# Kernel tuning notes

Measured on AMD Instinct MI355X. Metric: run time of the kernel, lower is better.

The kernel has to match this reference:

```python
import jax, jax.numpy as jnp
import numpy as np

B, P, D_IN = 128, 4096, 4   # frames, points/frame, xyz+time
NG = 16                      # number of trajectory groups
H1, H2, H3 = 64, 128, 512    # PointNet shared-MLP widths


def _init_mlp(key, dims):
    ks = jax.random.split(key, len(dims) - 1)
    params = []
    for k, (di, do) in zip(ks, zip(dims[:-1], dims[1:])):
        W = jax.random.normal(k, (di, do), dtype=jnp.float32) * (1.0 / np.sqrt(di))
        b = jnp.zeros((do,), dtype=jnp.float32)
        params.append((W, b))
    return params


def setup_inputs() -> dict:
    key = jax.random.key(0)
    k_pc, k_t, k_idx, k_g, k_l = jax.random.split(key, 5)
    pc = jax.random.normal(k_pc, (B, 3, P), dtype=jnp.float32)
    traj_time_batch = jax.random.uniform(k_t, (B, 1), dtype=jnp.float32)
    traj_inbatch_index = jnp.sort(jax.random.randint(k_idx, (B,), 0, NG)).astype(jnp.int32)
    (Wg1, bg1), (Wg2, bg2), (Wg3, bg3) = _init_mlp(k_g, [D_IN, H1, H2, H3])
    (Wl1, bl1), (Wl2, bl2), (Wl3, bl3) = _init_mlp(k_l, [D_IN, H1, H2, H3])
    return dict(pc=pc, traj_time_batch=traj_time_batch, traj_inbatch_index=traj_inbatch_index,
                Wg1=Wg1, bg1=bg1, Wg2=Wg2, bg2=bg2, Wg3=Wg3, bg3=bg3,
                Wl1=Wl1, bl1=bl1, Wl2=Wl2, bl2=bl2, Wl3=Wl3, bl3=bl3)


def _mlp(x, layers):
    # pointwise shared MLP: x [..., P, d_in] -> [..., P, d_out]
    for W, b in layers:
        x = jax.nn.relu(x @ W + b)
    return x


def reference(pc, traj_time_batch, traj_inbatch_index,
              Wg1, bg1, Wg2, bg2, Wg3, bg3,
              Wl1, bl1, Wl2, bl2, Wl3, bl3):
    b, _, p = pc.shape
    # append time channel: [B,3,P] + [B,1,P] -> [B,4,P]
    t = jnp.broadcast_to(traj_time_batch[..., None], (b, 1, p))
    feat = jnp.concatenate([pc, t], axis=1)
    x = jnp.swapaxes(feat, 1, 2)  # [B,P,4] points-last layout for pointwise MLP

    # global branch: shared MLP on every point, then max over all points of each trajectory group
    hg = _mlp(x, [(Wg1, bg1), (Wg2, bg2), (Wg3, bg3)])           # [B,P,H3]
    seg = jnp.repeat(traj_inbatch_index, p)                       # [B*P]
    gmax = jax.ops.segment_max(hg.reshape(b * p, -1), seg, num_segments=NG)  # [NG,H3]
    global_feat = gmax[traj_inbatch_index]                        # [B,H3] broadcast back per frame

    # local branch: per-frame PointNet encode (shared MLP + max over points)
    hl = _mlp(x, [(Wl1, bl1), (Wl2, bl2), (Wl3, bl3)])            # [B,P,H3]
    local_feat = hl.max(axis=1)                                   # [B,H3]

    z = jnp.concatenate([global_feat, local_feat], axis=1)        # [B,2*H3]
    input_features_vis = pc                                       # original pc (last dim == 4096, no slice)
    return (z, input_features_vis)
```

## Files before the change

### kernel.cpp

```cpp
#include <hip/hip_runtime.h>
#include <hip/hip_bf16.h>

#define NB   128
#define NP   4096
#define NGRP 16
#define C3   512

typedef __bf16 bf16x8 __attribute__((ext_vector_type(8)));
typedef __bf16 bf16x4 __attribute__((ext_vector_type(4)));
typedef float  f32x4  __attribute__((ext_vector_type(4)));

#define WS_W1T_G 0
#define WS_W1T_L 4096
#define WS_W2T_G 8192
#define WS_W2T_L 24576
#define WS_W3T_G 40960
#define WS_W3T_L 172032
#define WS_GMAX  303104

#define H1_S 72
#define H2_S 136

__global__ void prep_kernel(const float* __restrict__ Wg1, const float* __restrict__ Wg2,
                            const float* __restrict__ Wg3, const float* __restrict__ Wl1,
                            const float* __restrict__ Wl2, const float* __restrict__ Wl3,
                            float* __restrict__ out, char* __restrict__ ws) {
    int gid = blockIdx.x * blockDim.x + threadIdx.x;
    out[gid] = 0.0f;
    float* gmax = (float*)(ws + WS_GMAX);
    if (gid < NGRP * C3) gmax[gid] = 0.0f;
    __bf16* w1tg = (__bf16*)(ws + WS_W1T_G);
    __bf16* w1tl = (__bf16*)(ws + WS_W1T_L);
    __bf16* w2tg = (__bf16*)(ws + WS_W2T_G);
    __bf16* w2tl = (__bf16*)(ws + WS_W2T_L);
    __bf16* w3tg = (__bf16*)(ws + WS_W3T_G);
    __bf16* w3tl = (__bf16*)(ws + WS_W3T_L);
    if (gid < 64 * 32) {
        int ch = gid >> 5, k = gid & 31;
        w1tg[gid] = (k < 4) ? (__bf16)Wg1[k * 64 + ch] : (__bf16)0.0f;
        w1tl[gid] = (k < 4) ? (__bf16)Wl1[k * 64 + ch] : (__bf16)0.0f;
    }
    if (gid < 128 * 64) {
        int ch = gid >> 6, k = gid & 63;
        w2tg[gid] = (__bf16)Wg2[k * 128 + ch];
        w2tl[gid] = (__bf16)Wl2[k * 128 + ch];
    }
    if (gid < 512 * 128) {
        int ch = gid >> 7, k = gid & 127;
        w3tg[gid] = (__bf16)Wg3[k * 512 + ch];
        w3tl[gid] = (__bf16)Wl3[k * 512 + ch];
    }
}

__global__ __launch_bounds__(512, 2) void main_kernel(
    const float* __restrict__ pc, const float* __restrict__ tt, const int* __restrict__ idx,
    const float* __restrict__ bg1, const float* __restrict__ bg2, const float* __restrict__ bg3,
    const float* __restrict__ bl1, const float* __restrict__ bl2, const float* __restrict__ bl3,
    float* __restrict__ out, char* __restrict__ ws) {
    __shared__ __align__(16) char smem[78848];
    __bf16* h1 = (__bf16*)smem;
    __bf16* h2 = (__bf16*)(smem + 9216);

    const int tid    = threadIdx.x;
    const int lane   = tid & 63;
    const int wave   = tid >> 6;
    const int quad   = lane >> 4;
    const int l15    = lane & 15;
    const int branch = blockIdx.y;
    const int chunk  = blockIdx.x;
    const int frame  = chunk >> 2;
    const int p0     = (chunk & 3) * 1024;

    const __bf16* w1t = (const __bf16*)(ws + (branch ? WS_W1T_L : WS_W1T_G));
    const __bf16* w2t = (const __bf16*)(ws + (branch ? WS_W2T_L : WS_W2T_G));
    const __bf16* w3t = (const __bf16*)(ws + (branch ? WS_W3T_L : WS_W3T_G));
    const float* b1 = branch ? bl1 : bg1;
    const float* b2 = branch ? bl2 : bg2;
    const float* b3 = branch ? bl3 : bg3;

    const int ni1  = wave >> 1;
    const int mi1  = (wave & 1) * 2;
    const int chb2 = wave * 16;
    const int ch3  = wave * 64;

    bf16x8 a1[2];
    #pragma unroll
    for (int mm = 0; mm < 2; ++mm)
        a1[mm] = *(const bf16x8*)(w1t + ((mi1 + mm) * 16 + l15) * 32 + quad * 8);
    bf16x8 a2[2];
    #pragma unroll
    for (int ks = 0; ks < 2; ++ks)
        a2[ks] = *(const bf16x8*)(w2t + (chb2 + l15) * 64 + ks * 32 + quad * 8);
    bf16x8 aw[4][4];
    #pragma unroll
    for (int mi = 0; mi < 4; ++mi)
        #pragma unroll
        for (int ks = 0; ks < 4; ++ks)
            aw[mi][ks] = *(const bf16x8*)(w3t + (ch3 + mi * 16 + l15) * 128 + ks * 32 + quad * 8);

    float b1r[2][4], b2r[4];
    #pragma unroll
    for (int mm = 0; mm < 2; ++mm)
        #pragma unroll
        for (int r = 0; r < 4; ++r) b1r[mm][r] = b1[(mi1 + mm) * 16 + quad * 4 + r];
    #pragma unroll
    for (int r = 0; r < 4; ++r) b2r[r] = b2[chb2 + quad * 4 + r];

    const float tval = tt[frame];
    const f32x4 zf = {0.0f, 0.0f, 0.0f, 0.0f};
    f32x4 runmax[4];
    #pragma unroll
    for (int mi = 0; mi < 4; ++mi) runmax[mi] = (f32x4){-1e30f, -1e30f, -1e30f, -1e30f};

    const float* pcx = pc + (size_t)frame * 3 * NP;

    for (int m = 0; m < 4; ++m) {
        float xf[4][3];
        const int pb = p0 + m * 256 + ni1 * 16 + l15;
        #pragma unroll
        for (int s = 0; s < 4; ++s) {
            xf[s][0] = pcx[pb + s * 64];
            xf[s][1] = pcx[NP + pb + s * 64];
            xf[s][2] = pcx[2 * NP + pb + s * 64];
        }

        #pragma unroll
        for (int s = 0; s < 4; ++s) {
            bf16x8 xb;
            #pragma unroll
            for (int j = 0; j < 8; ++j) xb[j] = (__bf16)0.0f;
            if (quad == 0) {
                xb[0] = (__bf16)xf[s][0]; xb[1] = (__bf16)xf[s][1];
                xb[2] = (__bf16)xf[s][2]; xb[3] = (__bf16)tval;
            }
            #pragma unroll
            for (int mm = 0; mm < 2; ++mm) {
                f32x4 c = __builtin_amdgcn_mfma_f32_16x16x32_bf16(a1[mm], xb, zf, 0, 0, 0);
                bf16x4 pk;
                #pragma unroll
                for (int r = 0; r < 4; ++r) pk[r] = (__bf16)fmaxf(c[r] + b1r[mm][r], 0.0f);
                *(bf16x4*)(h1 + (ni1 * 16 + l15) * H1_S + (mi1 + mm) * 16 + quad * 4) = pk;
            }
            __syncthreads();
            #pragma unroll
            for (int ni = 0; ni < 4; ++ni) {
                bf16x8 q0 = *(const bf16x8*)(h1 + (ni * 16 + l15) * H1_S + quad * 8);
                bf16x8 q1 = *(const bf16x8*)(h1 + (ni * 16 + l15) * H1_S + 32 + quad * 8);
                f32x4 c = __builtin_amdgcn_mfma_f32_16x16x32_bf16(a2[0], q0, zf, 0, 0, 0);
                c = __builtin_amdgcn_mfma_f32_16x16x32_bf16(a2[1], q1, c, 0, 0, 0);
                bf16x4 pk;
                #pragma unroll
                for (int r = 0; r < 4; ++r) pk[r] = (__bf16)fmaxf(c[r] + b2r[r], 0.0f);
                *(bf16x4*)(h2 + (s * 64 + ni * 16 + l15) * H2_S + chb2 + quad * 4) = pk;
            }
            __syncthreads();
        }

        bf16x8 bh[4], bhn[4];
        #pragma unroll
        for (int ks = 0; ks < 4; ++ks)
            bh[ks] = *(const bf16x8*)(h2 + l15 * H2_S + ks * 32 + quad * 8);
        #pragma unroll 4
        for (int ni = 0; ni < 16; ++ni) {
            const int nin = (ni + 1) & 15;
            #pragma unroll
            for (int ks = 0; ks < 4; ++ks)
                bhn[ks] = *(const bf16x8*)(h2 + (nin * 16 + l15) * H2_S + ks * 32 + quad * 8);
            f32x4 acc[4];
            #pragma unroll
            for (int ks = 0; ks < 4; ++ks)
                #pragma unroll
                for (int mi = 0; mi < 4; ++mi)
                    acc[mi] = __builtin_amdgcn_mfma_f32_16x16x32_bf16(
                        aw[mi][ks], bh[ks], ks ? acc[mi] : zf, 0, 0, 0);
            #pragma unroll
            for (int mi = 0; mi < 4; ++mi)
                #pragma unroll
                for (int r = 0; r < 4; ++r)
                    runmax[mi][r] = fmaxf(runmax[mi][r], acc[mi][r]);
            #pragma unroll
            for (int ks = 0; ks < 4; ++ks) bh[ks] = bhn[ks];
        }
    }

    const int g = idx[frame];
    float* gmax = (float*)(ws + WS_GMAX);
    unsigned* dst = (branch == 0) ? (unsigned*)(gmax + g * C3)
                                  : (unsigned*)(out + frame * (2 * C3) + C3);
    #pragma unroll
    for (int mi = 0; mi < 4; ++mi) {
        f32x4 v = runmax[mi];
        #pragma unroll
        for (int d = 1; d < 16; d <<= 1) {
            #pragma unroll
            for (int r = 0; r < 4; ++r) v[r] = fmaxf(v[r], __shfl_xor(v[r], d));
        }
        if (l15 == 0) {
            #pragma unroll
            for (int r = 0; r < 4; ++r) {
                int ch = ch3 + mi * 16 + quad * 4 + r;
                float fv = fmaxf(v[r] + b3[ch], 0.0f);
                atomicMax(dst + ch, __float_as_uint(fv));
            }
        }
    }
}

__global__ void gather_kernel(const int* __restrict__ idx, const char* __restrict__ ws,
                              float* __restrict__ out) {
    int i = blockIdx.x * blockDim.x + threadIdx.x;
    int b = i >> 9, ch = i & 511;
    const float* gmax = (const float*)(ws + WS_GMAX);
    out[b * (2 * C3) + ch] = gmax[idx[b] * C3 + ch];
}

extern "C" void kernel_launch(void* const* d_in, const int* in_sizes, int n_in,
                              void* d_out, int out_size, void* d_ws, size_t ws_size,
                              hipStream_t stream) {
    const float* pc  = (const float*)d_in[0];
    const float* tt  = (const float*)d_in[1];
    const int*   idx = (const int*)d_in[2];
    const float* Wg1 = (const float*)d_in[3];  const float* bg1 = (const float*)d_in[4];
    const float* Wg2 = (const float*)d_in[5];  const float* bg2 = (const float*)d_in[6];
    const float* Wg3 = (const float*)d_in[7];  const float* bg3 = (const float*)d_in[8];
    const float* Wl1 = (const float*)d_in[9];  const float* bl1 = (const float*)d_in[10];
    const float* Wl2 = (const float*)d_in[11]; const float* bl2 = (const float*)d_in[12];
    const float* Wl3 = (const float*)d_in[13]; const float* bl3 = (const float*)d_in[14];
    float* out = (float*)d_out;
    char*  ws  = (char*)d_ws;

    hipMemcpyAsync(out + NB * 2 * C3, pc, (size_t)NB * 3 * NP * sizeof(float),
                   hipMemcpyDeviceToDevice, stream);
    prep_kernel<<<512, 256, 0, stream>>>(Wg1, Wg2, Wg3, Wl1, Wl2, Wl3, out, ws);
    main_kernel<<<dim3(512, 2), 512, 0, stream>>>(pc, tt, idx, bg1, bg2, bg3,
                                                  bl1, bl2, bl3, out, ws);
    gather_kernel<<<256, 256, 0, stream>>>(idx, ws, out);
}
```

Before: 233.0 us.

## Use fragment-native LDS layout for activations and fold pc copy into prep

Activation tiles h1/h2 in shared memory move from padded row-major storage to a layout laid out in MFMA B-operand fragment order. Each lane can then read its bf16x8 operand contiguously at lane*8, with no padding and fewer bank conflicts. Separately, the device-to-device hipMemcpyAsync of pc into the output is replaced by a vectorized copy inside prep_kernel, which removes one launch and copy operation. The trade-off is more complex index math on the writes, and prep_kernel now does extra memory traffic.

```diff
diff --git a/kernel.cpp b/kernel.cpp
--- a/kernel.cpp
+++ b/kernel.cpp
@@ -9,6 +9,7 @@
 typedef __bf16 bf16x8 __attribute__((ext_vector_type(8)));
 typedef __bf16 bf16x4 __attribute__((ext_vector_type(4)));
 typedef float  f32x4  __attribute__((ext_vector_type(4)));
+typedef float  float4v __attribute__((ext_vector_type(4)));
 
 #define WS_W1T_G 0
 #define WS_W1T_L 4096
@@ -18,15 +19,19 @@
 #define WS_W3T_L 172032
 #define WS_GMAX  303104
 
-#define H1_S 72
-#define H2_S 136
-
 __global__ void prep_kernel(const float* __restrict__ Wg1, const float* __restrict__ Wg2,
                             const float* __restrict__ Wg3, const float* __restrict__ Wl1,
                             const float* __restrict__ Wl2, const float* __restrict__ Wl3,
+                            const float* __restrict__ pc,
                             float* __restrict__ out, char* __restrict__ ws) {
     int gid = blockIdx.x * blockDim.x + threadIdx.x;
     out[gid] = 0.0f;
+    {
+        const float4v* src = (const float4v*)pc;
+        float4v* dst = (float4v*)(out + NB * 2 * C3);
+        #pragma unroll
+        for (int j = 0; j < 3; ++j) dst[j * 131072 + gid] = src[j * 131072 + gid];
+    }
     float* gmax = (float*)(ws + WS_GMAX);
     if (gid < NGRP * C3) gmax[gid] = 0.0f;
     __bf16* w1tg = (__bf16*)(ws + WS_W1T_G);
@@ -57,9 +62,9 @@
     const float* __restrict__ bg1, const float* __restrict__ bg2, const float* __restrict__ bg3,
     const float* __restrict__ bl1, const float* __restrict__ bl2, const float* __restrict__ bl3,
     float* __restrict__ out, char* __restrict__ ws) {
-    __shared__ __align__(16) char smem[78848];
-    __bf16* h1 = (__bf16*)smem;
-    __bf16* h2 = (__bf16*)(smem + 9216);
+    __shared__ __align__(16) char smem[73728];
+    __bf16* h1f = (__bf16*)smem;
+    __bf16* h2f = (__bf16*)(smem + 8192);
 
     const int tid    = threadIdx.x;
     const int lane   = tid & 63;
@@ -114,6 +119,10 @@
 
     const float* pcx = pc + (size_t)frame * 3 * NP;
 
+    const int w2ks = wave >> 1;
+    const int w2qk = (wave & 1) * 2 + (quad >> 1);
+    const int j0   = (quad & 1) * 4;
+
     for (int m = 0; m < 4; ++m) {
         float xf[4][3];
         const int pb = p0 + m * 256 + ni1 * 16 + l15;
@@ -139,19 +148,22 @@
                 bf16x4 pk;
                 #pragma unroll
                 for (int r = 0; r < 4; ++r) pk[r] = (__bf16)fmaxf(c[r] + b1r[mm][r], 0.0f);
-                *(bf16x4*)(h1 + (ni1 * 16 + l15) * H1_S + (mi1 + mm) * 16 + quad * 4) = pk;
+                const int cks = (mi1 + mm) >> 1;
+                const int cqk = ((mi1 + mm) & 1) * 2 + (quad >> 1);
+                *(bf16x4*)(h1f + ((ni1 * 2 + cks) * 4 + cqk) * 128 + l15 * 8 + j0) = pk;
             }
             __syncthreads();
             #pragma unroll
             for (int ni = 0; ni < 4; ++ni) {
-                bf16x8 q0 = *(const bf16x8*)(h1 + (ni * 16 + l15) * H1_S + quad * 8);
-                bf16x8 q1 = *(const bf16x8*)(h1 + (ni * 16 + l15) * H1_S + 32 + quad * 8);
+                bf16x8 q0 = *(const bf16x8*)(h1f + (ni * 2 + 0) * 512 + lane * 8);
+                bf16x8 q1 = *(const bf16x8*)(h1f + (ni * 2 + 1) * 512 + lane * 8);
                 f32x4 c = __builtin_amdgcn_mfma_f32_16x16x32_bf16(a2[0], q0, zf, 0, 0, 0);
                 c = __builtin_amdgcn_mfma_f32_16x16x32_bf16(a2[1], q1, c, 0, 0, 0);
                 bf16x4 pk;
                 #pragma unroll
                 for (int r = 0; r < 4; ++r) pk[r] = (__bf16)fmaxf(c[r] + b2r[r], 0.0f);
-                *(bf16x4*)(h2 + (s * 64 + ni * 16 + l15) * H2_S + chb2 + quad * 4) = pk;
+                const int pni = s * 4 + ni;
+                *(bf16x4*)(h2f + ((pni * 4 + w2ks) * 4 + w2qk) * 128 + l15 * 8 + j0) = pk;
             }
             __syncthreads();
         }
@@ -159,13 +171,13 @@
         bf16x8 bh[4], bhn[4];
         #pragma unroll
         for (int ks = 0; ks < 4; ++ks)
-            bh[ks] = *(const bf16x8*)(h2 + l15 * H2_S + ks * 32 + quad * 8);
+            bh[ks] = *(const bf16x8*)(h2f + ks * 512 + lane * 8);
         #pragma unroll 4
         for (int ni = 0; ni < 16; ++ni) {
             const int nin = (ni + 1) & 15;
             #pragma unroll
             for (int ks = 0; ks < 4; ++ks)
-                bhn[ks] = *(const bf16x8*)(h2 + (nin * 16 + l15) * H2_S + ks * 32 + quad * 8);
+                bhn[ks] = *(const bf16x8*)(h2f + (nin * 4 + ks) * 512 + lane * 8);
             f32x4 acc[4];
             #pragma unroll
             for (int ks = 0; ks < 4; ++ks)
@@ -229,9 +241,7 @@
     float* out = (float*)d_out;
     char*  ws  = (char*)d_ws;
 
-    hipMemcpyAsync(out + NB * 2 * C3, pc, (size_t)NB * 3 * NP * sizeof(float),
-                   hipMemcpyDeviceToDevice, stream);
-    prep_kernel<<<512, 256, 0, stream>>>(Wg1, Wg2, Wg3, Wl1, Wl2, Wl3, out, ws);
+    prep_kernel<<<512, 256, 0, stream>>>(Wg1, Wg2, Wg3, Wl1, Wl2, Wl3, pc, out, ws);
     main_kernel<<<dim3(512, 2), 512, 0, stream>>>(pc, tt, idx, bg1, bg2, bg3,
                                                   bl1, bl2, bl3, out, ws);
     gather_kernel<<<256, 256, 0, stream>>>(idx, ws, out);
```

Result: faster. 228.3 us (-2.0%).
